# Kernel tuning notes

Measured on AMD Instinct MI355X. Metric: run time of the kernel, lower is better.

## Reference

```python
import jax, jax.numpy as jnp
import numpy as np

S, O, T, C, H = 32, 64, 91, 128, 8  # scenes, objects, timesteps, dim, heads


def setup_inputs() -> dict:
    key = jax.random.key(0)
    ks = jax.random.split(key, 6)
    x = jax.random.normal(ks[0], (S, O, T, C), dtype=jnp.float32)
    valid_mask = jax.random.randint(ks[1], (S, O, T), 0, 2) > 0

    def lin(k, shape):
        return jax.random.normal(k, shape, dtype=jnp.float32) / np.float32(np.sqrt(shape[-1]))

    return dict(
        x=x,
        valid_mask=valid_mask,
        Wqkv_a=lin(ks[2], (3 * C, C)), Wproj_a=lin(ks[3], (C, C)), bproj_a=jnp.zeros((C,), jnp.float32),
        Wqkv_t=lin(ks[4], (3 * C, C)), Wproj_t=lin(ks[5], (C, C)), bproj_t=jnp.zeros((C,), jnp.float32),
    )


def _masked_mha(x, mask, Wqkv, Wproj, bproj):
    # x: (B, N, C); mask: (B, N, N) bool. qkv has no bias, proj has bias.
    B, N, Cd = x.shape
    hd = Cd // H
    scale = hd ** (-0.5)
    qkv = (x @ Wqkv.T).reshape(B, N, 3, H, hd).transpose(2, 0, 3, 1, 4)
    q, k, v = qkv[0], qkv[1], qkv[2]  # (B, H, N, hd)
    s = jnp.einsum('bhnd,bhmd->bhnm', q, k) * scale
    s = jnp.where(mask[:, None], s, -jnp.inf)
    # rows that are fully masked are set to all-zeros (-> uniform softmax), as in torch code
    dead = jnp.all(~mask, axis=-1)  # (B, N)
    s = jnp.where(dead[:, None, :, None], jnp.float32(0.0), s)
    a = jax.nn.softmax(s, axis=-1)
    o = jnp.einsum('bhnm,bhmd->bhnd', a, v).transpose(0, 2, 1, 3).reshape(B, N, Cd)
    return o @ Wproj.T + bproj


def reference(x, valid_mask, Wqkv_a, Wproj_a, bproj_a, Wqkv_t, Wproj_t, bproj_t):
    S_, O_, T_, C_ = x.shape
    # agent-wise attention: attend across objects at each (scene, timestep)
    xa = x.transpose(0, 2, 1, 3).reshape(S_ * T_, O_, C_)
    ma = valid_mask.transpose(0, 2, 1)  # (S, T, O)
    ma = (ma[..., :, None] & ma[..., None, :]).reshape(S_ * T_, O_, O_)
    xa = _masked_mha(xa, ma, Wqkv_a, Wproj_a, bproj_a)
    # time-wise attention: attend across timesteps for each (scene, object)
    xt = xa.reshape(S_, T_, O_, C_).transpose(0, 2, 1, 3).reshape(S_ * O_, T_, C_)
    mt = (valid_mask[..., :, None] & valid_mask[..., None, :]).reshape(S_ * O_, T_, T_)
    xt = _masked_mha(xt, mt, Wqkv_t, Wproj_t, bproj_t)
    return xt.reshape(S_, O_, T_, C_)
```

## Files before the change

### kernel.cpp

```cpp
#include <hip/hip_runtime.h>

#define S_ 32
#define O_ 64
#define T_ 91
#define C_ 128
#define H_ 8
#define HD_ 16

typedef __attribute__((ext_vector_type(8))) short short8;
typedef __attribute__((ext_vector_type(4))) short short4b;
typedef __attribute__((ext_vector_type(4))) float f32x4;

__device__ __forceinline__ void splitf(float f, short& h, short& l) {
    unsigned u = __float_as_uint(f);
    float hf = __uint_as_float(u & 0xffff0000u);
    h = (short)(u >> 16);
    l = (short)(__float_as_uint(f - hf) >> 16);
}

__device__ __forceinline__ void split8g(const float* p, short8& h, short8& l) {
    float4 a = *(const float4*)p;
    float4 b = *(const float4*)(p + 4);
    float v[8] = {a.x, a.y, a.z, a.w, b.x, b.y, b.z, b.w};
    #pragma unroll
    for (int j = 0; j < 8; ++j) { short hh, ll; splitf(v[j], hh, ll); h[j] = hh; l[j] = ll; }
}

__device__ __forceinline__ void split4v(f32x4 v, short4b& h, short4b& l) {
    #pragma unroll
    for (int j = 0; j < 4; ++j) { short hh, ll; splitf(v[j], hh, ll); h[j] = hh; l[j] = ll; }
}

template<int N, int NT>
__global__ __launch_bounds__(512) void fused_pass(
    const float* __restrict__ xg, const int* __restrict__ mask,
    const float* __restrict__ Wqkv, const float* __restrict__ Wproj,
    const float* __restrict__ bproj, float* __restrict__ yout,
    int bdiv, long bs1, long bs2, long ts, long m1, long m2)
{
    constexpr bool FULL = (NT * 16 == N);
    extern __shared__ char smem[];
    short* xh = (short*)smem;
    short* xl = xh + NT * 2048;
    float* ylds = (float*)smem;
    int*   s_m = (int*)(smem + NT * 8704);

    const int tid = threadIdx.x;
    const int wv = tid >> 6, l = tid & 63;
    const int ic = l & 15, g = l >> 4;
    const int b = blockIdx.x;
    const int s = b / bdiv, u = b - s * bdiv;
    const long xbase = (long)s * bs1 + (long)u * bs2;
    const long mbase = (long)s * (O_ * T_) + (long)u * m1;

    for (int gi = tid; gi < NT * 256; gi += 512) {
        int token = gi >> 4, cg = gi & 15;
        int kp = cg >> 2, gg = cg & 3;
        int slot = ((token >> 4) * 4 + kp) * 512 + (gg * 16 + (token & 15)) * 8;
        short8 vh, vl;
        if (FULL || token < N) {
            const float* p = xg + xbase + (long)token * ts + cg * 8;
            split8g(p, vh, vl);
        } else {
            #pragma unroll
            for (int j = 0; j < 8; ++j) { vh[j] = 0; vl[j] = 0; }
        }
        *(short8*)(xh + slot) = vh;
        *(short8*)(xl + slot) = vl;
    }
    for (int idx = tid; idx < NT * 16; idx += 512)
        s_m[idx] = (idx < N) ? (mask[mbase + (long)idx * m2] != 0) : 0;
    __syncthreads();

    unsigned jbits = 0, mbits = 0;
    #pragma unroll
    for (int jt = 0; jt < NT; ++jt)
        #pragma unroll
        for (int r = 0; r < 4; ++r) {
            int j = jt * 16 + 4 * g + r;
            if (j < N) {
                jbits |= 1u << (jt * 4 + r);
                if (s_m[j]) mbits |= 1u << (jt * 4 + r);
            }
        }

    const int h = wv;
    const float* Wqp = Wqkv + (long)(h * 16 + ic) * C_;
    const float* Wkp = Wqkv + (long)(128 + h * 16 + ic) * C_;
    const float* Wvp = Wqkv + (long)(256 + h * 16 + ic) * C_;

    f32x4 aQ[NT], aK[NT], aV[NT];
    #pragma unroll
    for (int t = 0; t < NT; ++t) {
        aQ[t] = (f32x4){0.f,0.f,0.f,0.f};
        aK[t] = (f32x4){0.f,0.f,0.f,0.f};
        aV[t] = (f32x4){0.f,0.f,0.f,0.f};
    }
    #pragma unroll
    for (int kp = 0; kp < 4; ++kp) {
        short8 wqh, wql, wkh, wkl, wvh, wvl;
        split8g(Wqp + kp * 32 + g * 8, wqh, wql);
        split8g(Wkp + kp * 32 + g * 8, wkh, wkl);
        split8g(Wvp + kp * 32 + g * 8, wvh, wvl);
        #pragma unroll
        for (int tt = 0; tt < NT; ++tt) {
            short8 xhv = *(const short8*)(xh + (tt * 4 + kp) * 512 + l * 8);
            short8 xlv = *(const short8*)(xl + (tt * 4 + kp) * 512 + l * 8);
            aQ[tt] = __builtin_amdgcn_mfma_f32_16x16x32_bf16(wqh, xhv, aQ[tt], 0, 0, 0);
            aQ[tt] = __builtin_amdgcn_mfma_f32_16x16x32_bf16(wql, xhv, aQ[tt], 0, 0, 0);
            aQ[tt] = __builtin_amdgcn_mfma_f32_16x16x32_bf16(wqh, xlv, aQ[tt], 0, 0, 0);
            aK[tt] = __builtin_amdgcn_mfma_f32_16x16x32_bf16(wkh, xhv, aK[tt], 0, 0, 0);
            aK[tt] = __builtin_amdgcn_mfma_f32_16x16x32_bf16(wkl, xhv, aK[tt], 0, 0, 0);
            aK[tt] = __builtin_amdgcn_mfma_f32_16x16x32_bf16(wkh, xlv, aK[tt], 0, 0, 0);
            aV[tt] = __builtin_amdgcn_mfma_f32_16x16x32_bf16(xhv, wvh, aV[tt], 0, 0, 0);
            aV[tt] = __builtin_amdgcn_mfma_f32_16x16x32_bf16(xlv, wvh, aV[tt], 0, 0, 0);
            aV[tt] = __builtin_amdgcn_mfma_f32_16x16x32_bf16(xhv, wvl, aV[tt], 0, 0, 0);
        }
    }
    short4b qfh[NT], qfl[NT], kfh[NT], kfl[NT], vfh[NT], vfl[NT];
    #pragma unroll
    for (int t = 0; t < NT; ++t) {
        split4v(aQ[t], qfh[t], qfl[t]);
        split4v(aK[t], kfh[t], kfl[t]);
        split4v(aV[t], vfh[t], vfl[t]);
    }
    __syncthreads();

    for (int it = 0; it < NT; ++it) {
        f32x4 sa[NT];
        #pragma unroll
        for (int jt = 0; jt < NT; ++jt) sa[jt] = (f32x4){0.f,0.f,0.f,0.f};
        #pragma unroll
        for (int jt = 0; jt < NT; ++jt) {
            sa[jt] = __builtin_amdgcn_mfma_f32_16x16x16bf16_1k(kfh[jt], qfh[it], sa[jt], 0, 0, 0);
            sa[jt] = __builtin_amdgcn_mfma_f32_16x16x16bf16_1k(kfl[jt], qfh[it], sa[jt], 0, 0, 0);
            sa[jt] = __builtin_amdgcn_mfma_f32_16x16x16bf16_1k(kfh[jt], qfl[it], sa[jt], 0, 0, 0);
        }
        const int query = it * 16 + ic;
        const bool iok = FULL || (query < N);
        const int qm = iok ? s_m[query] : 0;

        float sum = 0.f;
        short4b ph[NT], pl[NT];
        #pragma unroll
        for (int jt = 0; jt < NT; ++jt) {
            #pragma unroll
            for (int r = 0; r < 4; ++r) {
                int bit = (jt << 2) + r;
                float e;
                if (!iok) e = 0.f;
                else if (!qm) e = ((jbits >> bit) & 1) ? 1.f : 0.f;
                else e = ((mbits >> bit) & 1) ? __expf(sa[jt][r] * 0.25f) : 0.f;
                sum += e;
                short hh, ll; splitf(e, hh, ll);
                ph[jt][r] = hh; pl[jt][r] = ll;
            }
        }
        sum += __shfl_xor(sum, 16, 64);
        sum += __shfl_xor(sum, 32, 64);
        const float inv = 1.f / sum;

        f32x4 pv = (f32x4){0.f,0.f,0.f,0.f};
        #pragma unroll
        for (int kt = 0; kt < NT; ++kt) {
            pv = __builtin_amdgcn_mfma_f32_16x16x16bf16_1k(ph[kt], vfh[kt], pv, 0, 0, 0);
            pv = __builtin_amdgcn_mfma_f32_16x16x16bf16_1k(pl[kt], vfh[kt], pv, 0, 0, 0);
            pv = __builtin_amdgcn_mfma_f32_16x16x16bf16_1k(ph[kt], vfl[kt], pv, 0, 0, 0);
        }
        #pragma unroll
        for (int r = 0; r < 4; ++r) {
            int rloc = 4 * g + r;
            int row = it * 16 + rloc;
            int iv = __builtin_amdgcn_ds_bpermute(rloc << 2, __float_as_int(inv));
            if (FULL || row < N)
                ylds[row * 136 + h * 16 + ic] = pv[r] * __int_as_float(iv);
        }
    }
    __syncthreads();

    const float* Wpr = Wproj + (long)(wv * 16 + ic) * C_;
    short8 pwh[4], pwl[4];
    #pragma unroll
    for (int kp = 0; kp < 4; ++kp) split8g(Wpr + kp * 32 + g * 8, pwh[kp], pwl[kp]);
    const float bv = bproj[wv * 16 + ic];

    #pragma unroll
    for (int mt = 0; mt < NT; ++mt) {
        f32x4 acc = (f32x4){0.f,0.f,0.f,0.f};
        #pragma unroll
        for (int kp = 0; kp < 4; ++kp) {
            const float* yp = ylds + (mt * 16 + ic) * 136 + kp * 32 + g * 8;
            short8 ayh, ayl;
            split8g(yp, ayh, ayl);
            acc = __builtin_amdgcn_mfma_f32_16x16x32_bf16(ayh, pwh[kp], acc, 0, 0, 0);
            acc = __builtin_amdgcn_mfma_f32_16x16x32_bf16(ayl, pwh[kp], acc, 0, 0, 0);
            acc = __builtin_amdgcn_mfma_f32_16x16x32_bf16(ayh, pwl[kp], acc, 0, 0, 0);
        }
        #pragma unroll
        for (int r = 0; r < 4; ++r) {
            int row = mt * 16 + 4 * g + r;
            if (FULL || row < N)
                yout[((long)b * N + row) * C_ + wv * 16 + ic] = acc[r] + bv;
        }
    }
}

extern "C" void kernel_launch(void* const* d_in, const int* in_sizes, int n_in,
                              void* d_out, int out_size, void* d_ws, size_t ws_size,
                              hipStream_t stream) {
    const float* x       = (const float*)d_in[0];
    const int*   mask    = (const int*)d_in[1];
    const float* Wqkv_a  = (const float*)d_in[2];
    const float* Wproj_a = (const float*)d_in[3];
    const float* bproj_a = (const float*)d_in[4];
    const float* Wqkv_t  = (const float*)d_in[5];
    const float* Wproj_t = (const float*)d_in[6];
    const float* bproj_t = (const float*)d_in[7];
    float* out = (float*)d_out;
    float* xa  = (float*)d_ws;

    {
        const size_t lds = 4 * 8704 + 4 * 64;
        fused_pass<O_, 4><<<S_ * T_, 512, lds, stream>>>(
            x, mask, Wqkv_a, Wproj_a, bproj_a, xa,
            T_, (long)O_ * T_ * C_, (long)C_, (long)T_ * C_,
            1L, (long)T_);
    }
    {
        const size_t lds = 6 * 8704 + 6 * 64;
        fused_pass<T_, 6><<<S_ * O_, 512, lds, stream>>>(
            xa, mask, Wqkv_t, Wproj_t, bproj_t, out,
            O_, (long)T_ * O_ * C_, (long)C_, (long)O_ * C_,
            (long)T_, 1L);
    }
}
```

Before: 328.8 us.

## Pre-split weights to bf16 hi/lo once, drop P-lo MFMA, store y pre-split

Adds a prep kernel that splits all weight matrices into bf16 hi/lo pairs in MFMA fragment layout, so each fused block loads them directly instead of re-splitting fp32 weights. The softmax folds the scale and log2e into Q, uses exp2 with a select-based mask, and rounds P to a single bf16, which removes one of the three PV MFMAs. The attention output is written to LDS already split into hi/lo fragments, avoiding an fp32 staging buffer and its re-split, and the attention loop is unrolled. Rounding P to one bf16 term lowers accuracy of the PV product.

```diff
diff --git a/kernel.cpp b/kernel.cpp
--- a/kernel.cpp
+++ b/kernel.cpp
@@ -5,11 +5,15 @@
 #define T_ 91
 #define C_ 128
 #define H_ 8
-#define HD_ 16
 
 typedef __attribute__((ext_vector_type(8))) short short8;
 typedef __attribute__((ext_vector_type(4))) short short4b;
 typedef __attribute__((ext_vector_type(4))) float f32x4;
+
+__device__ short g_wqa_h[384 * 128], g_wqa_l[384 * 128];
+__device__ short g_wqt_h[384 * 128], g_wqt_l[384 * 128];
+__device__ short g_wpa_h[128 * 128], g_wpa_l[128 * 128];
+__device__ short g_wpt_h[128 * 128], g_wpt_l[128 * 128];
 
 __device__ __forceinline__ void splitf(float f, short& h, short& l) {
     unsigned u = __float_as_uint(f);
@@ -31,10 +35,30 @@
     for (int j = 0; j < 4; ++j) { short hh, ll; splitf(v[j], hh, ll); h[j] = hh; l[j] = ll; }
 }
 
-template<int N, int NT>
+__global__ __launch_bounds__(256) void prep_all(
+    const float* __restrict__ wqa, const float* __restrict__ wqt,
+    const float* __restrict__ wpa, const float* __restrict__ wpt)
+{
+    int t = blockIdx.x * 256 + threadIdx.x;
+    const float* src; short* dh; short* dl; int idx;
+    if (t < 6144)       { src = wqa; dh = g_wqa_h; dl = g_wqa_l; idx = t; }
+    else if (t < 12288) { src = wqt; dh = g_wqt_h; dl = g_wqt_l; idx = t - 6144; }
+    else if (t < 14336) { src = wpa; dh = g_wpa_h; dl = g_wpa_l; idx = t - 12288; }
+    else                { src = wpt; dh = g_wpt_h; dl = g_wpt_l; idx = t - 14336; }
+    int c = idx >> 4, gk = idx & 15;
+    int kp = gk >> 2, gg = gk & 3;
+    int ct = c >> 4, cl = c & 15;
+    const float* s = src + (long)c * C_ + gk * 8;
+    long slot = (long)ct * 2048 + kp * 512 + (cl + 16 * gg) * 8;
+    short8 vh, vl;
+    split8g(s, vh, vl);
+    *(short8*)(dh + slot) = vh;
+    *(short8*)(dl + slot) = vl;
+}
+
+template<int N, int NT, int PASS>
 __global__ __launch_bounds__(512) void fused_pass(
     const float* __restrict__ xg, const int* __restrict__ mask,
-    const float* __restrict__ Wqkv, const float* __restrict__ Wproj,
     const float* __restrict__ bproj, float* __restrict__ yout,
     int bdiv, long bs1, long bs2, long ts, long m1, long m2)
 {
@@ -42,8 +66,14 @@
     extern __shared__ char smem[];
     short* xh = (short*)smem;
     short* xl = xh + NT * 2048;
-    float* ylds = (float*)smem;
-    int*   s_m = (int*)(smem + NT * 8704);
+    short* yh = xh;
+    short* yl = xl;
+    int*   s_m = (int*)(smem + NT * 8192);
+
+    const short* Wh = (PASS == 0) ? g_wqa_h : g_wqt_h;
+    const short* Wl = (PASS == 0) ? g_wqa_l : g_wqt_l;
+    const short* Ph = (PASS == 0) ? g_wpa_h : g_wpt_h;
+    const short* Pl = (PASS == 0) ? g_wpa_l : g_wpt_l;
 
     const int tid = threadIdx.x;
     const int wv = tid >> 6, l = tid & 63;
@@ -59,8 +89,7 @@
         int slot = ((token >> 4) * 4 + kp) * 512 + (gg * 16 + (token & 15)) * 8;
         short8 vh, vl;
         if (FULL || token < N) {
-            const float* p = xg + xbase + (long)token * ts + cg * 8;
-            split8g(p, vh, vl);
+            split8g(xg + xbase + (long)token * ts + cg * 8, vh, vl);
         } else {
             #pragma unroll
             for (int j = 0; j < 8; ++j) { vh[j] = 0; vl[j] = 0; }
@@ -85,23 +114,21 @@
         }
 
     const int h = wv;
-    const float* Wqp = Wqkv + (long)(h * 16 + ic) * C_;
-    const float* Wkp = Wqkv + (long)(128 + h * 16 + ic) * C_;
-    const float* Wvp = Wqkv + (long)(256 + h * 16 + ic) * C_;
-
     f32x4 aQ[NT], aK[NT], aV[NT];
     #pragma unroll
-    for (int t = 0; t < NT; ++t) {
-        aQ[t] = (f32x4){0.f,0.f,0.f,0.f};
-        aK[t] = (f32x4){0.f,0.f,0.f,0.f};
-        aV[t] = (f32x4){0.f,0.f,0.f,0.f};
+    for (int t2 = 0; t2 < NT; ++t2) {
+        aQ[t2] = (f32x4){0.f,0.f,0.f,0.f};
+        aK[t2] = (f32x4){0.f,0.f,0.f,0.f};
+        aV[t2] = (f32x4){0.f,0.f,0.f,0.f};
     }
     #pragma unroll
     for (int kp = 0; kp < 4; ++kp) {
-        short8 wqh, wql, wkh, wkl, wvh, wvl;
-        split8g(Wqp + kp * 32 + g * 8, wqh, wql);
-        split8g(Wkp + kp * 32 + g * 8, wkh, wkl);
-        split8g(Wvp + kp * 32 + g * 8, wvh, wvl);
+        short8 wqh = *(const short8*)(Wh + (h * 4 + kp) * 512 + l * 8);
+        short8 wql = *(const short8*)(Wl + (h * 4 + kp) * 512 + l * 8);
+        short8 wkh = *(const short8*)(Wh + ((8 + h) * 4 + kp) * 512 + l * 8);
+        short8 wkl = *(const short8*)(Wl + ((8 + h) * 4 + kp) * 512 + l * 8);
+        short8 wvh = *(const short8*)(Wh + ((16 + h) * 4 + kp) * 512 + l * 8);
+        short8 wvl = *(const short8*)(Wl + ((16 + h) * 4 + kp) * 512 + l * 8);
         #pragma unroll
         for (int tt = 0; tt < NT; ++tt) {
             short8 xhv = *(const short8*)(xh + (tt * 4 + kp) * 512 + l * 8);
@@ -117,15 +144,28 @@
             aV[tt] = __builtin_amdgcn_mfma_f32_16x16x32_bf16(xhv, wvl, aV[tt], 0, 0, 0);
         }
     }
+    const float QS = 0.25f * 1.44269504088896f;
     short4b qfh[NT], qfl[NT], kfh[NT], kfl[NT], vfh[NT], vfl[NT];
     #pragma unroll
-    for (int t = 0; t < NT; ++t) {
-        split4v(aQ[t], qfh[t], qfl[t]);
-        split4v(aK[t], kfh[t], kfl[t]);
-        split4v(aV[t], vfh[t], vfl[t]);
+    for (int t2 = 0; t2 < NT; ++t2) {
+        f32x4 qs = aQ[t2] * QS;
+        split4v(qs, qfh[t2], qfl[t2]);
+        split4v(aK[t2], kfh[t2], kfl[t2]);
+        split4v(aV[t2], vfh[t2], vfl[t2]);
+    }
+    short8 pwh[4], pwl[4];
+    #pragma unroll
+    for (int kp = 0; kp < 4; ++kp) {
+        pwh[kp] = *(const short8*)(Ph + (wv * 4 + kp) * 512 + l * 8);
+        pwl[kp] = *(const short8*)(Pl + (wv * 4 + kp) * 512 + l * 8);
     }
     __syncthreads();
 
+    const int kpw = wv >> 1;
+    const int ggw = (2 * wv + (ic >> 3)) & 3;
+    const int jw  = ic & 7;
+
+    #pragma unroll
     for (int it = 0; it < NT; ++it) {
         f32x4 sa[NT];
         #pragma unroll
@@ -137,23 +177,22 @@
             sa[jt] = __builtin_amdgcn_mfma_f32_16x16x16bf16_1k(kfh[jt], qfl[it], sa[jt], 0, 0, 0);
         }
         const int query = it * 16 + ic;
-        const bool iok = FULL || (query < N);
-        const int qm = iok ? s_m[query] : 0;
-
+        const int qm = s_m[query];
+        const unsigned msel = qm ? mbits : jbits;
         float sum = 0.f;
-        short4b ph[NT], pl[NT];
+        short4b ph[NT];
         #pragma unroll
         for (int jt = 0; jt < NT; ++jt) {
             #pragma unroll
             for (int r = 0; r < 4; ++r) {
                 int bit = (jt << 2) + r;
-                float e;
-                if (!iok) e = 0.f;
-                else if (!qm) e = ((jbits >> bit) & 1) ? 1.f : 0.f;
-                else e = ((mbits >> bit) & 1) ? __expf(sa[jt][r] * 0.25f) : 0.f;
+                float inner = qm ? sa[jt][r] : 0.f;
+                float xv = ((msel >> bit) & 1u) ? inner : -1e30f;
+                float e = exp2f(xv);
                 sum += e;
-                short hh, ll; splitf(e, hh, ll);
-                ph[jt][r] = hh; pl[jt][r] = ll;
+                unsigned ue = __float_as_uint(e);
+                ue += 0x7fffu + ((ue >> 16) & 1u);
+                ph[jt][r] = (short)(ue >> 16);
             }
         }
         sum += __shfl_xor(sum, 16, 64);
@@ -164,7 +203,6 @@
         #pragma unroll
         for (int kt = 0; kt < NT; ++kt) {
             pv = __builtin_amdgcn_mfma_f32_16x16x16bf16_1k(ph[kt], vfh[kt], pv, 0, 0, 0);
-            pv = __builtin_amdgcn_mfma_f32_16x16x16bf16_1k(pl[kt], vfh[kt], pv, 0, 0, 0);
             pv = __builtin_amdgcn_mfma_f32_16x16x16bf16_1k(ph[kt], vfl[kt], pv, 0, 0, 0);
         }
         #pragma unroll
@@ -172,26 +210,24 @@
             int rloc = 4 * g + r;
             int row = it * 16 + rloc;
             int iv = __builtin_amdgcn_ds_bpermute(rloc << 2, __float_as_int(inv));
-            if (FULL || row < N)
-                ylds[row * 136 + h * 16 + ic] = pv[r] * __int_as_float(iv);
+            float yv = pv[r] * __int_as_float(iv);
+            short hh = 0, ll = 0;
+            if (FULL || row < N) splitf(yv, hh, ll);
+            int slot = (it * 4 + kpw) * 512 + (ggw * 16 + rloc) * 8 + jw;
+            yh[slot] = hh;
+            yl[slot] = ll;
         }
     }
     __syncthreads();
 
-    const float* Wpr = Wproj + (long)(wv * 16 + ic) * C_;
-    short8 pwh[4], pwl[4];
-    #pragma unroll
-    for (int kp = 0; kp < 4; ++kp) split8g(Wpr + kp * 32 + g * 8, pwh[kp], pwl[kp]);
     const float bv = bproj[wv * 16 + ic];
-
     #pragma unroll
     for (int mt = 0; mt < NT; ++mt) {
         f32x4 acc = (f32x4){0.f,0.f,0.f,0.f};
         #pragma unroll
         for (int kp = 0; kp < 4; ++kp) {
-            const float* yp = ylds + (mt * 16 + ic) * 136 + kp * 32 + g * 8;
-            short8 ayh, ayl;
-            split8g(yp, ayh, ayl);
+            short8 ayh = *(const short8*)(yh + (mt * 4 + kp) * 512 + l * 8);
+            short8 ayl = *(const short8*)(yl + (mt * 4 + kp) * 512 + l * 8);
             acc = __builtin_amdgcn_mfma_f32_16x16x32_bf16(ayh, pwh[kp], acc, 0, 0, 0);
             acc = __builtin_amdgcn_mfma_f32_16x16x32_bf16(ayl, pwh[kp], acc, 0, 0, 0);
             acc = __builtin_amdgcn_mfma_f32_16x16x32_bf16(ayh, pwl[kp], acc, 0, 0, 0);
@@ -211,25 +247,27 @@
     const float* x       = (const float*)d_in[0];
     const int*   mask    = (const int*)d_in[1];
     const float* Wqkv_a  = (const float*)d_in[2];
-    const float* Wproj_a = (const float*)d_in[3];
     const float* bproj_a = (const float*)d_in[4];
     const float* Wqkv_t  = (const float*)d_in[5];
+    const float* bproj_t = (const float*)d_in[7];
+    const float* Wproj_a = (const float*)d_in[3];
     const float* Wproj_t = (const float*)d_in[6];
-    const float* bproj_t = (const float*)d_in[7];
     float* out = (float*)d_out;
     float* xa  = (float*)d_ws;
 
+    prep_all<<<64, 256, 0, stream>>>(Wqkv_a, Wqkv_t, Wproj_a, Wproj_t);
+
     {
-        const size_t lds = 4 * 8704 + 4 * 64;
-        fused_pass<O_, 4><<<S_ * T_, 512, lds, stream>>>(
-            x, mask, Wqkv_a, Wproj_a, bproj_a, xa,
+        const size_t lds = 4 * 8192 + 4 * 64;
+        fused_pass<O_, 4, 0><<<S_ * T_, 512, lds, stream>>>(
+            x, mask, bproj_a, xa,
             T_, (long)O_ * T_ * C_, (long)C_, (long)T_ * C_,
             1L, (long)T_);
     }
     {
-        const size_t lds = 6 * 8704 + 6 * 64;
-        fused_pass<T_, 6><<<S_ * O_, 512, lds, stream>>>(
-            xa, mask, Wqkv_t, Wproj_t, bproj_t, out,
+        const size_t lds = 6 * 8192 + 6 * 64;
+        fused_pass<T_, 6, 1><<<S_ * O_, 512, lds, stream>>>(
+            xa, mask, bproj_t, out,
             O_, (long)T_ * O_ * C_, (long)C_, (long)O_ * C_,
             (long)T_, 1L);
     }
```

After: 313.7 us. 4.6% less time.
